# Kernel tuning notes

Measured on AMD Instinct MI355X. Metric: run time of the kernel, lower is better.

The kernel has to match this reference:

```python
import jax, jax.numpy as jnp
import numpy as np


def setup_inputs() -> dict:
    key = jax.random.key(0)
    k1, k2, k3, k4 = jax.random.split(key, 4)
    B, Cin, Cout, N, modes = 16, 128, 128, 8192, 64
    scale = 1.0 / (Cin * Cout)
    x = jax.random.normal(k1, (B, Cin, N), dtype=jnp.float32)
    # spectral weight: [in, out, modes, 2] uniform in [0, scale) like torch.rand * scale
    w_spec = scale * jax.random.uniform(k2, (Cin, Cout, modes, 2), dtype=jnp.float32)
    # Conv1d(kernel=1) weight [out, in] and bias [out] (kaiming-uniform-ish init)
    bound = 1.0 / np.sqrt(Cin)
    w_conv = jax.random.uniform(k3, (Cout, Cin), minval=-bound, maxval=bound, dtype=jnp.float32)
    b_conv = jax.random.uniform(k4, (Cout,), minval=-bound, maxval=bound, dtype=jnp.float32)
    return {"x": x, "w_spec": w_spec, "w_conv": w_conv, "b_conv": b_conv}


def reference(x, w_spec, w_conv, b_conv):
    N = x.shape[-1]
    modes = w_spec.shape[2]
    n_freq = N // 2 + 1
    # Spectral conv: rfft, keep first `modes` coefficients, complex channel mix
    x_ft = jnp.fft.rfft(x)  # [B, Cin, n_freq] complex64
    w_c = w_spec[..., 0] + 1j * w_spec[..., 1]  # [Cin, Cout, modes]
    out_m = jnp.einsum('bim,iom->bom', x_ft[:, :, :modes], w_c)  # [B, Cout, modes]
    out_ft = jnp.pad(out_m, ((0, 0), (0, 0), (0, n_freq - modes)))
    x1 = jnp.fft.irfft(out_ft, n=N)  # [B, Cout, N]
    # 1x1 conv (pointwise channel mix)
    x2 = jnp.einsum('bin,oi->bon', x, w_conv) + b_conv[None, :, None]
    return jax.nn.gelu(x1 + x2, approximate=False)
```

## Files before the change

### kernel.cpp

```cpp
#include <hip/hip_runtime.h>
#include <hip/hip_bf16.h>
#include <math.h>

#define NB    16
#define NCIN  128
#define NCOUT 128
#define NN    8192
#define NMOD  64

typedef short bf16x8 __attribute__((ext_vector_type(8)));
typedef float f32x4  __attribute__((ext_vector_type(4)));

#define MFMA16(a, b, c) __builtin_amdgcn_mfma_f32_16x16x32_bf16((a), (b), (c), 0, 0, 0)

__device__ inline unsigned short f2bf_rne(float f) {
    unsigned u = __float_as_uint(f);
    u += 0x7FFF + ((u >> 16) & 1);
    return (unsigned short)(u >> 16);
}
__device__ inline short f2bf_trunc(float f) {
    return (short)(__float_as_uint(f) >> 16);
}

__global__ __launch_bounds__(256) void k_prep(const float* __restrict__ wc,
                                              const float* __restrict__ wsp,
                                              unsigned short* __restrict__ T,
                                              unsigned short* __restrict__ Tt,
                                              unsigned short* __restrict__ Wcb,
                                              unsigned short* __restrict__ Wpk) {
    const float C = 7.66990393943e-4f;
    if (blockIdx.x < 16) {
        int a = blockIdx.x * 256 + threadIdx.x;
        int k = a >> 6, n0 = (a & 63) * 128;
        for (int j8 = 0; j8 < 16; ++j8) {
            short c8[8], s8[8];
            #pragma unroll
            for (int j = 0; j < 8; ++j) {
                int n = n0 + j8 * 8 + j;
                int ph = (k * n) & (NN - 1);
                float sn, cs; __sincosf((float)ph * C, &sn, &cs);
                c8[j] = (short)f2bf_rne(cs);
                s8[j] = (short)f2bf_rne(-sn);
            }
            *(bf16x8*)(T + (size_t)(2 * k) * NN + n0 + j8 * 8)     = *(bf16x8*)c8;
            *(bf16x8*)(T + (size_t)(2 * k + 1) * NN + n0 + j8 * 8) = *(bf16x8*)s8;
        }
    } else if (blockIdx.x < 48) {
        int n = (blockIdx.x - 16) * 256 + threadIdx.x;
        for (int k4 = 0; k4 < 16; ++k4) {
            short buf[8];
            #pragma unroll
            for (int j = 0; j < 4; ++j) {
                int k = k4 * 4 + j;
                int ph = (n * k) & (NN - 1);
                float sn, cs; __sincosf((float)ph * C, &sn, &cs);
                buf[2 * j]     = (short)f2bf_rne(cs);
                buf[2 * j + 1] = (short)f2bf_rne(-sn);
            }
            *(bf16x8*)(Tt + (size_t)n * 128 + k4 * 8) = *(bf16x8*)buf;
        }
    } else if (blockIdx.x < 112) {
        int j = (blockIdx.x - 48) * 256 + threadIdx.x;
        if (j < NCOUT * NCIN) Wcb[j] = f2bf_rne(wc[j]);
    } else {
        int g2 = (blockIdx.x - 112) * 256 + threadIdx.x;
        int k  = g2 & 63;
        int o  = (g2 >> 6) & 127;
        int ch = g2 >> 13;
        const float s = (k == 0) ? (1.f / NN) : (2.f / NN);
        const float2* wp = (const float2*)wsp;
        unsigned short* wre = Wpk + ((size_t)(k * 2 + 0) * 128 + o) * 256;
        unsigned short* wim = Wpk + ((size_t)(k * 2 + 1) * 128 + o) * 256;
        for (int c = ch * 8; c < ch * 8 + 8; ++c) {
            int i0 = 4 * c;
            short re8[8], im8[8];
            #pragma unroll
            for (int t2 = 0; t2 < 4; ++t2) {
                float2 wv = wp[((size_t)(i0 + t2) * 128 + o) * 64 + k];
                float wr = s * wv.x, wi = s * wv.y;
                re8[2 * t2]     = (short)f2bf_rne(wr);
                re8[2 * t2 + 1] = (short)f2bf_rne(-wi);
                im8[2 * t2]     = (k == 0) ? (short)0 : (short)f2bf_rne(wi);
                im8[2 * t2 + 1] = (k == 0) ? (short)0 : (short)f2bf_rne(wr);
            }
            *(bf16x8*)(wre + c * 8) = *(bf16x8*)re8;
            *(bf16x8*)(wim + c * 8) = *(bf16x8*)im8;
        }
    }
}

__global__ __launch_bounds__(256) void k_dftmm(const float* __restrict__ x,
                                               const unsigned short* __restrict__ T,
                                               float* __restrict__ Cpart) {
    const int mt = blockIdx.x & 63, sp = blockIdx.x >> 6;
    const int w = threadIdx.x >> 6, l = threadIdx.x & 63;
    const int l15 = l & 15, q = l >> 4;
    const int colbase = w * 32;
    f32x4 acc[2][2] = {};
    for (int kt = 0; kt < 16; ++kt) {
        const int kb = sp * 512 + kt * 32;
        bf16x8 a[2], bb[2];
        #pragma unroll
        for (int mf = 0; mf < 2; ++mf) {
            const float* ap = x + (size_t)(mt * 32 + mf * 16 + l15) * NN + kb + q * 8;
            float4 f0 = *(const float4*)ap;
            float4 f1 = *(const float4*)(ap + 4);
            short t8[8] = { f2bf_trunc(f0.x), f2bf_trunc(f0.y), f2bf_trunc(f0.z), f2bf_trunc(f0.w),
                            f2bf_trunc(f1.x), f2bf_trunc(f1.y), f2bf_trunc(f1.z), f2bf_trunc(f1.w) };
            a[mf] = *(bf16x8*)t8;
        }
        #pragma unroll
        for (int nf = 0; nf < 2; ++nf)
            bb[nf] = *(const bf16x8*)(T + (size_t)(colbase + nf * 16 + l15) * NN + kb + q * 8);
        #pragma unroll
        for (int mf = 0; mf < 2; ++mf) {
            acc[mf][0] = MFMA16(a[mf], bb[0], acc[mf][0]);
            acc[mf][1] = MFMA16(a[mf], bb[1], acc[mf][1]);
        }
    }
    #pragma unroll
    for (int mf = 0; mf < 2; ++mf)
        #pragma unroll
        for (int nf = 0; nf < 2; ++nf) {
            int col  = colbase + nf * 16 + l15;
            int row0 = mt * 32 + mf * 16 + q * 4;
            *(f32x4*)(Cpart + (size_t)sp * 262144 + (size_t)col * 2048 + row0) = acc[mf][nf];
        }
}

__global__ __launch_bounds__(256) void k_reduce(const float* __restrict__ Cpart,
                                                float* __restrict__ Xf) {
    int t = blockIdx.x * 256 + threadIdx.x;
    float s = 0.f;
    #pragma unroll
    for (int sp = 0; sp < 16; ++sp) s += Cpart[(size_t)sp * 262144 + t];
    Xf[t] = s;
}

__global__ __launch_bounds__(64) void k_mixmm(const float* __restrict__ Xf,
                                              const unsigned short* __restrict__ Wpk,
                                              unsigned short* __restrict__ Aspec) {
    const int k = blockIdx.x >> 2, oq = blockIdx.x & 3;
    const int l = threadIdx.x, l15 = l & 15, q = l >> 4;
    f32x4 ar[2] = {}, ai[2] = {};
    const float* xr = Xf + (size_t)(2 * k) * 2048 + l15 * 128;
    const float* xi = xr + 2048;
    #pragma unroll
    for (int kt = 0; kt < 8; ++kt) {
        int i0 = kt * 16 + q * 4;
        float4 r4 = *(const float4*)(xr + i0);
        float4 i4 = *(const float4*)(xi + i0);
        short a8[8] = { (short)f2bf_rne(r4.x), (short)f2bf_rne(i4.x),
                        (short)f2bf_rne(r4.y), (short)f2bf_rne(i4.y),
                        (short)f2bf_rne(r4.z), (short)f2bf_rne(i4.z),
                        (short)f2bf_rne(r4.w), (short)f2bf_rne(i4.w) };
        bf16x8 a = *(bf16x8*)a8;
        #pragma unroll
        for (int nf = 0; nf < 2; ++nf) {
            int o = oq * 32 + nf * 16 + l15;
            const unsigned short* wb = Wpk + ((size_t)(k * 2) * 128 + o) * 256 + kt * 32 + q * 8;
            bf16x8 bre = *(const bf16x8*)wb;
            bf16x8 bim = *(const bf16x8*)(wb + 32768);
            ar[nf] = MFMA16(a, bre, ar[nf]);
            ai[nf] = MFMA16(a, bim, ai[nf]);
        }
    }
    #pragma unroll
    for (int nf = 0; nf < 2; ++nf) {
        int o = oq * 32 + nf * 16 + l15;
        #pragma unroll
        for (int r = 0; r < 4; ++r) {
            int b = q * 4 + r;
            unsigned v = (unsigned)f2bf_rne(ar[nf][r]) | ((unsigned)f2bf_rne(ai[nf][r]) << 16);
            *(unsigned*)(Aspec + ((size_t)b * 128 + o) * 128 + 2 * k) = v;
        }
    }
}

__global__ __launch_bounds__(256) void k_out(const float* __restrict__ x,
                                             const unsigned short* __restrict__ Tt,
                                             const unsigned short* __restrict__ Aspec,
                                             const unsigned short* __restrict__ Wcb,
                                             const float* __restrict__ bias,
                                             float* __restrict__ out) {
    const int b = blockIdx.x >> 7, nt = blockIdx.x & 127;
    const int w = threadIdx.x >> 6, l = threadIdx.x & 63;
    const int l15 = l & 15, q = l >> 4;
    const int wo = w >> 1, wn = w & 1;
    __shared__ short xs[8192];

    const float* xb = x + (size_t)b * 128 * NN + nt * 64;
    #pragma unroll
    for (int it = 0; it < 4; ++it) {
        int unit = it * 256 + threadIdx.x;
        int ipair = unit >> 4, nq = unit & 15;
        int i0 = ipair * 2;
        const float* p0 = xb + (size_t)i0 * NN + nq * 4;
        float4 r0 = *(const float4*)p0;
        float4 r1 = *(const float4*)(p0 + NN);
        float a0[4] = { r0.x, r0.y, r0.z, r0.w };
        float a1[4] = { r1.x, r1.y, r1.z, r1.w };
        #pragma unroll
        for (int j = 0; j < 4; ++j) {
            int n = nq * 4 + j;
            unsigned v = (unsigned)(unsigned short)f2bf_trunc(a0[j])
                       | ((unsigned)(unsigned short)f2bf_trunc(a1[j]) << 16);
            int swz = (n ^ (n >> 2)) & 15;
            int addr = n * 128 + (((i0 >> 3) ^ swz) * 8) + (i0 & 7);
            *(unsigned*)&xs[addr] = v;
        }
    }

    const int obase = wo * 64;
    const int nbase = nt * 64 + wn * 32;
    f32x4 acc[4][2] = {};
    #pragma unroll
    for (int kt = 0; kt < 4; ++kt) {
        bf16x8 bb[2];
        #pragma unroll
        for (int nf = 0; nf < 2; ++nf) {
            int n = nbase + nf * 16 + l15;
            bb[nf] = *(const bf16x8*)(Tt + (size_t)n * 128 + kt * 32 + q * 8);
        }
        const unsigned short* Ap = Aspec + (size_t)b * 16384 + kt * 32 + q * 8;
        #pragma unroll
        for (int mf = 0; mf < 4; ++mf) {
            bf16x8 a = *(const bf16x8*)(Ap + (size_t)(obase + mf * 16 + l15) * 128);
            acc[mf][0] = MFMA16(a, bb[0], acc[mf][0]);
            acc[mf][1] = MFMA16(a, bb[1], acc[mf][1]);
        }
    }
    __syncthreads();
    #pragma unroll
    for (int kt = 0; kt < 4; ++kt) {
        bf16x8 bb[2];
        #pragma unroll
        for (int nf = 0; nf < 2; ++nf) {
            int nl = wn * 32 + nf * 16 + l15;
            int c  = kt * 4 + q;
            int swz = (nl ^ (nl >> 2)) & 15;
            bb[nf] = *(const bf16x8*)&xs[nl * 128 + ((c ^ swz) * 8)];
        }
        const unsigned short* Ap = Wcb + kt * 32 + q * 8;
        #pragma unroll
        for (int mf = 0; mf < 4; ++mf) {
            bf16x8 a = *(const bf16x8*)(Ap + (size_t)(obase + mf * 16 + l15) * 128);
            acc[mf][0] = MFMA16(a, bb[0], acc[mf][0]);
            acc[mf][1] = MFMA16(a, bb[1], acc[mf][1]);
        }
    }
    #pragma unroll
    for (int mf = 0; mf < 4; ++mf)
        #pragma unroll
        for (int nf = 0; nf < 2; ++nf)
            #pragma unroll
            for (int r = 0; r < 4; ++r) {
                int o = obase + mf * 16 + q * 4 + r;
                int n = nbase + nf * 16 + l15;
                float v = acc[mf][nf][r] + bias[o];
                float u = v * v;
                float p = v * fmaf(0.0713548162f, u, 1.5957691216f);
                float e = __expf(-p);
                float g = v * __builtin_amdgcn_rcpf(1.f + e);
                out[((size_t)(b * 128 + o)) * NN + n] = g;
            }
}

extern "C" void kernel_launch(void* const* d_in, const int* in_sizes, int n_in,
                              void* d_out, int out_size, void* d_ws, size_t ws_size,
                              hipStream_t stream) {
    const float* x    = (const float*)d_in[0];
    const float* wsp  = (const float*)d_in[1];
    const float* wc   = (const float*)d_in[2];
    const float* bc   = (const float*)d_in[3];
    float* out = (float*)d_out;

    unsigned short* T   = (unsigned short*)d_ws;
    unsigned short* Tt  = T + (size_t)1048576;
    unsigned short* Wcb = Tt + (size_t)1048576;
    unsigned short* Asp = Wcb + 16384;
    unsigned short* Wpk = Asp + 262144;
    float* Cpart = (float*)(Wpk + (size_t)8388608);
    float* Xf    = Cpart + (size_t)16 * 262144;

    k_prep  <<<240,  256, 0, stream>>>(wc, wsp, T, Tt, Wcb, Wpk);
    k_dftmm <<<1024, 256, 0, stream>>>(x, T, Cpart);
    k_reduce<<<1024, 256, 0, stream>>>(Cpart, Xf);
    k_mixmm <<<256,  64,  0, stream>>>(Xf, Wpk, Asp);
    k_out   <<<2048, 256, 0, stream>>>(x, Tt, Asp, Wcb, bc, out);
}
```

Baseline: 227.9 us.

## Stage x tiles in swizzled LDS with double buffering in DFT matmul; split mixmm finer

In the DFT GEMM kernel, each block now loads its 32-row x slice cooperatively with coalesced 16-float loads, converts it to bf16 and stores it into an XOR-swizzled shared-memory double buffer. The next chunk is prefetched into registers while MFMAs run on the current one, replacing per-wave strided global loads that four waves each repeated for the same x rows. The mixing kernel is split into twice as many blocks, each computing one 16-wide output tile, to raise parallelism. The cost is extra LDS use and barriers per chunk in the DFT kernel, and less register reuse of the A fragment in mixmm.

```diff
diff --git a/kernel.cpp b/kernel.cpp
--- a/kernel.cpp
+++ b/kernel.cpp
@@ -96,28 +96,61 @@
     const int w = threadIdx.x >> 6, l = threadIdx.x & 63;
     const int l15 = l & 15, q = l >> 4;
     const int colbase = w * 32;
+    __shared__ short As[8192];
+
+    const int sr = threadIdx.x >> 3;
+    const int sc = threadIdx.x & 7;
+    const float* xrow = x + (size_t)(mt * 32 + sr) * NN + sp * 512 + sc * 16;
+    short* wp0 = As + sr * 128 + (((sc * 2    ) ^ (sr & 7)) * 8);
+    short* wp1 = As + sr * 128 + (((sc * 2 + 1) ^ (sr & 7)) * 8);
+
+    float4 ra, rb, rc, rd;
+#define LOADC(c) { const float* p_ = xrow + (c) * 128;                         \
+        ra = *(const float4*)p_;       rb = *(const float4*)(p_ + 4);          \
+        rc = *(const float4*)(p_ + 8); rd = *(const float4*)(p_ + 12); }
+#define WRITEC(bufi) {                                                          \
+        short t0_[8] = { f2bf_trunc(ra.x), f2bf_trunc(ra.y), f2bf_trunc(ra.z), f2bf_trunc(ra.w), \
+                         f2bf_trunc(rb.x), f2bf_trunc(rb.y), f2bf_trunc(rb.z), f2bf_trunc(rb.w) }; \
+        short t1_[8] = { f2bf_trunc(rc.x), f2bf_trunc(rc.y), f2bf_trunc(rc.z), f2bf_trunc(rc.w), \
+                         f2bf_trunc(rd.x), f2bf_trunc(rd.y), f2bf_trunc(rd.z), f2bf_trunc(rd.w) }; \
+        *(bf16x8*)(wp0 + (bufi) * 4096) = *(bf16x8*)t0_;                        \
+        *(bf16x8*)(wp1 + (bufi) * 4096) = *(bf16x8*)t1_; }
+
+    const unsigned short* Tp0 = T + (size_t)(colbase + l15) * NN + sp * 512 + q * 8;
+    const unsigned short* Tp1 = Tp0 + (size_t)16 * NN;
+
+    const int rsw = l15 & 7;
+
+    LOADC(0);
+    WRITEC(0);
+    __syncthreads();
+
     f32x4 acc[2][2] = {};
-    for (int kt = 0; kt < 16; ++kt) {
-        const int kb = sp * 512 + kt * 32;
-        bf16x8 a[2], bb[2];
-        #pragma unroll
-        for (int mf = 0; mf < 2; ++mf) {
-            const float* ap = x + (size_t)(mt * 32 + mf * 16 + l15) * NN + kb + q * 8;
-            float4 f0 = *(const float4*)ap;
-            float4 f1 = *(const float4*)(ap + 4);
-            short t8[8] = { f2bf_trunc(f0.x), f2bf_trunc(f0.y), f2bf_trunc(f0.z), f2bf_trunc(f0.w),
-                            f2bf_trunc(f1.x), f2bf_trunc(f1.y), f2bf_trunc(f1.z), f2bf_trunc(f1.w) };
-            a[mf] = *(bf16x8*)t8;
-        }
-        #pragma unroll
-        for (int nf = 0; nf < 2; ++nf)
-            bb[nf] = *(const bf16x8*)(T + (size_t)(colbase + nf * 16 + l15) * NN + kb + q * 8);
-        #pragma unroll
-        for (int mf = 0; mf < 2; ++mf) {
-            acc[mf][0] = MFMA16(a[mf], bb[0], acc[mf][0]);
-            acc[mf][1] = MFMA16(a[mf], bb[1], acc[mf][1]);
-        }
-    }
+    int buf = 0;
+    for (int c = 0; c < 4; ++c) {
+        if (c < 3) LOADC(c + 1);
+        const short* Ab = As + buf * 4096;
+        #pragma unroll
+        for (int kk = 0; kk < 4; ++kk) {
+            int ce = ((kk * 4 + q) ^ rsw) * 8;
+            bf16x8 a0 = *(const bf16x8*)(Ab + l15 * 128 + ce);
+            bf16x8 a1 = *(const bf16x8*)(Ab + (16 + l15) * 128 + ce);
+            bf16x8 b0 = *(const bf16x8*)(Tp0 + c * 128 + kk * 32);
+            bf16x8 b1 = *(const bf16x8*)(Tp1 + c * 128 + kk * 32);
+            acc[0][0] = MFMA16(a0, b0, acc[0][0]);
+            acc[0][1] = MFMA16(a0, b1, acc[0][1]);
+            acc[1][0] = MFMA16(a1, b0, acc[1][0]);
+            acc[1][1] = MFMA16(a1, b1, acc[1][1]);
+        }
+        if (c < 3) {
+            WRITEC(buf ^ 1);
+            __syncthreads();
+            buf ^= 1;
+        }
+    }
+#undef LOADC
+#undef WRITEC
+
     #pragma unroll
     for (int mf = 0; mf < 2; ++mf)
         #pragma unroll
@@ -140,11 +173,12 @@
 __global__ __launch_bounds__(64) void k_mixmm(const float* __restrict__ Xf,
                                               const unsigned short* __restrict__ Wpk,
                                               unsigned short* __restrict__ Aspec) {
-    const int k = blockIdx.x >> 2, oq = blockIdx.x & 3;
+    const int k = blockIdx.x >> 3, oq = blockIdx.x & 7;
     const int l = threadIdx.x, l15 = l & 15, q = l >> 4;
-    f32x4 ar[2] = {}, ai[2] = {};
+    f32x4 ar = {}, ai = {};
     const float* xr = Xf + (size_t)(2 * k) * 2048 + l15 * 128;
     const float* xi = xr + 2048;
+    const int o = oq * 16 + l15;
     #pragma unroll
     for (int kt = 0; kt < 8; ++kt) {
         int i0 = kt * 16 + q * 4;
@@ -155,25 +189,17 @@
                         (short)f2bf_rne(r4.z), (short)f2bf_rne(i4.z),
                         (short)f2bf_rne(r4.w), (short)f2bf_rne(i4.w) };
         bf16x8 a = *(bf16x8*)a8;
-        #pragma unroll
-        for (int nf = 0; nf < 2; ++nf) {
-            int o = oq * 32 + nf * 16 + l15;
-            const unsigned short* wb = Wpk + ((size_t)(k * 2) * 128 + o) * 256 + kt * 32 + q * 8;
-            bf16x8 bre = *(const bf16x8*)wb;
-            bf16x8 bim = *(const bf16x8*)(wb + 32768);
-            ar[nf] = MFMA16(a, bre, ar[nf]);
-            ai[nf] = MFMA16(a, bim, ai[nf]);
-        }
-    }
-    #pragma unroll
-    for (int nf = 0; nf < 2; ++nf) {
-        int o = oq * 32 + nf * 16 + l15;
-        #pragma unroll
-        for (int r = 0; r < 4; ++r) {
-            int b = q * 4 + r;
-            unsigned v = (unsigned)f2bf_rne(ar[nf][r]) | ((unsigned)f2bf_rne(ai[nf][r]) << 16);
-            *(unsigned*)(Aspec + ((size_t)b * 128 + o) * 128 + 2 * k) = v;
-        }
+        const unsigned short* wb = Wpk + ((size_t)(k * 2) * 128 + o) * 256 + kt * 32 + q * 8;
+        bf16x8 bre = *(const bf16x8*)wb;
+        bf16x8 bim = *(const bf16x8*)(wb + 32768);
+        ar = MFMA16(a, bre, ar);
+        ai = MFMA16(a, bim, ai);
+    }
+    #pragma unroll
+    for (int r = 0; r < 4; ++r) {
+        int b = q * 4 + r;
+        unsigned v = (unsigned)f2bf_rne(ar[r]) | ((unsigned)f2bf_rne(ai[r]) << 16);
+        *(unsigned*)(Aspec + ((size_t)b * 128 + o) * 128 + 2 * k) = v;
     }
 }
 
@@ -286,6 +312,6 @@
     k_prep  <<<240,  256, 0, stream>>>(wc, wsp, T, Tt, Wcb, Wpk);
     k_dftmm <<<1024, 256, 0, stream>>>(x, T, Cpart);
     k_reduce<<<1024, 256, 0, stream>>>(Cpart, Xf);
-    k_mixmm <<<256,  64,  0, stream>>>(Xf, Wpk, Asp);
+    k_mixmm <<<512,  64,  0, stream>>>(Xf, Wpk, Asp);
     k_out   <<<2048, 256, 0, stream>>>(x, Tt, Asp, Wcb, bc, out);
 }
```

Measured after the change: 197.9 us. -13.2%, faster.
